# Kernel tuning notes

Measured on AMD Instinct MI355X. Metric: run time of the kernel, lower is better.

## Reference

```python
import jax, jax.numpy as jnp
import numpy as np
from jax import lax

B, T, H, L, IN = 256, 512, 128, 128, 3


def setup_inputs() -> dict:
    key = jax.random.key(0)
    ks = jax.random.split(key, 24)
    def n(k, shape, s=0.05):
        return jax.random.normal(k, shape, dtype=jnp.float32) * s
    lengths = jax.random.randint(ks[0], (B,), T // 2, T + 1)
    masks = (jnp.arange(T)[None, :] < lengths[:, None]).astype(jnp.int32)
    return {
        "x": n(ks[1], (B, T, IN), 1.0),
        "y": n(ks[2], (B, L, IN), 1.0),
        "masks": masks,
        "lengths": lengths,
        "W_ih0": n(ks[3], (4 * H, IN)), "W_hh0": n(ks[4], (4 * H, H)),
        "b_ih0": n(ks[5], (4 * H,)), "b_hh0": n(ks[6], (4 * H,)),
        "W_ih1": n(ks[7], (4 * H, H)), "W_hh1": n(ks[8], (4 * H, H)),
        "b_ih1": n(ks[9], (4 * H,)), "b_hh1": n(ks[10], (4 * H,)),
        "Wa": n(ks[11], (H, H)), "bWa": n(ks[12], (H,)),
        "Ua": n(ks[13], (H, H)), "bUa": n(ks[14], (H,)),
        "Va": n(ks[15], (H,)), "bVa": n(ks[16], (1,)),
        "fc1_w": n(ks[17], (32, H)), "fc1_b": n(ks[18], (32,)),
        "fc2_w": n(ks[19], (2, 32)), "fc2_b": n(ks[20], (2,)),
    }


def _lstm_cell(x_t, h, c, Wih, Whh, bih, bhh):
    # PyTorch gate order: i, f, g, o
    g = x_t @ Wih.T + h @ Whh.T + bih + bhh
    i, f, gg, o = jnp.split(g, 4, axis=-1)
    c = jax.nn.sigmoid(f) * c + jax.nn.sigmoid(i) * jnp.tanh(gg)
    h = jax.nn.sigmoid(o) * jnp.tanh(c)
    return h, c


def reference(x, y, masks, lengths,
              W_ih0, W_hh0, b_ih0, b_hh0,
              W_ih1, W_hh1, b_ih1, b_hh1,
              Wa, bWa, Ua, bUa, Va, bVa,
              fc1_w, fc1_b, fc2_w, fc2_b):
    Bn, Tn, _ = x.shape
    Ln = y.shape[1]
    Hn = W_hh0.shape[1]
    z = jnp.zeros((Bn, Hn), x.dtype)

    # ---- encoder: 2-layer LSTM with pack_padded semantics ----
    valid = (jnp.arange(Tn)[:, None] < lengths[None, :])[..., None]  # (T,B,1)

    def enc_step(carry, inp):
        h1, c1, h2, c2 = carry
        x_t, v = inp
        h1n, c1n = _lstm_cell(x_t, h1, c1, W_ih0, W_hh0, b_ih0, b_hh0)
        h2n, c2n = _lstm_cell(h1n, h2, c2, W_ih1, W_hh1, b_ih1, b_hh1)
        h1 = jnp.where(v, h1n, h1); c1 = jnp.where(v, c1n, c1)
        h2 = jnp.where(v, h2n, h2); c2 = jnp.where(v, c2n, c2)
        return (h1, c1, h2, c2), jnp.where(v, h2n, 0.0)

    (h1, c1, h2, c2), outs = lax.scan(enc_step, (z, z, z, z),
                                      (x.transpose(1, 0, 2), valid))
    lstm_out = outs.transpose(1, 0, 2)  # (B,T,H), zeros past length

    def attention(lo, h, m):
        s = jnp.tanh(lo @ Wa.T + bWa + (h @ Ua.T + bUa)[:, None, :])  # (B,T,H)
        scores = s @ Va + bVa  # (B,T)
        scores = jnp.where(m == 0, -jnp.inf, scores)
        w = jax.nn.softmax(scores, axis=1)
        return jnp.einsum('bt,btd->bd', w, lo)

    def head(ctx):
        return jax.nn.relu(ctx @ fc1_w.T + fc1_b) @ fc2_w.T + fc2_b

    out0 = head(attention(lstm_out, h2, masks))  # (B,2)

    # ---- decode loop (training=True, sampling_prob=1.0 -> pure teacher forcing) ----
    def dec_step(carry, inp):
        h1, c1, h2, c2, lo, m = carry
        y_t, i = inp
        h1, c1 = _lstm_cell(y_t, h1, c1, W_ih0, W_hh0, b_ih0, b_hh0)
        h2, c2 = _lstm_cell(h1, h2, c2, W_ih1, W_hh1, b_ih1, b_hh1)
        lo = lo.at[:, i + 1].set(h2)
        m = m.at[:, i + 1].set(1)
        out = head(attention(lo, h2, m))
        return (h1, c1, h2, c2, lo, m), out

    _, outs_dec = lax.scan(dec_step, (h1, c1, h2, c2, lstm_out, masks),
                           (y[:, :Ln - 1].transpose(1, 0, 2), jnp.arange(Ln - 1)))
    outputs = jnp.concatenate([out0[:, None, :], outs_dec.transpose(1, 0, 2)], axis=1)
    return outputs  # (B, L, 2)
```

## Files before the change

### kernel.cpp

```cpp
#include <hip/hip_runtime.h>

#define T 512
#define HDIM 128
#define LOUT 128
#define KEXT 639
#define KPAD 640
#define BM 4

typedef _Float16 half8 __attribute__((ext_vector_type(8)));
typedef _Float16 half4 __attribute__((ext_vector_type(4)));
typedef _Float16 half2t __attribute__((ext_vector_type(2)));
typedef float f32x4 __attribute__((ext_vector_type(4)));
typedef unsigned int u32x4 __attribute__((ext_vector_type(4)));

__device__ __forceinline__ int clampT(int v) { return v < 0 ? 0 : (v > T ? T : v); }

__device__ __forceinline__ half8 load8f(const float* p) {
  float4 q0 = *(const float4*)p;
  float4 q1 = *(const float4*)(p + 4);
  half8 v;
  v[0] = (_Float16)q0.x; v[1] = (_Float16)q0.y; v[2] = (_Float16)q0.z; v[3] = (_Float16)q0.w;
  v[4] = (_Float16)q1.x; v[5] = (_Float16)q1.y; v[6] = (_Float16)q1.z; v[7] = (_Float16)q1.w;
  return v;
}

__device__ __forceinline__ half8 load8h_once(const _Float16* p) {
  u32x4 raw = *(volatile const u32x4*)p;
  return __builtin_bit_cast(half8, raw);
}

__device__ __forceinline__ void cell_up(float gi, float gf, float gg, float go,
                                        float& cr, _Float16& hh, bool v) {
  const float A = 1.44269504f, B2 = 2.88539008f;
  const float Fi = __builtin_amdgcn_exp2f(-gi * A);
  const float Ff = __builtin_amdgcn_exp2f(-gf * A);
  const float Fo = __builtin_amdgcn_exp2f(-go * A);
  const float Eg = __builtin_amdgcn_exp2f(gg * B2);
  const float it = (Eg - 1.f) * __builtin_amdgcn_rcpf((1.f + Fi) * (1.f + Eg));
  const float cn = cr * __builtin_amdgcn_rcpf(1.f + Ff) + it;
  const float ec = __builtin_amdgcn_exp2f(-B2 * __builtin_fabsf(cn));
  const float h  = __builtin_copysignf(
      (1.f - ec) * __builtin_amdgcn_rcpf((1.f + Fo) * (1.f + ec)), cn);
  if (v) { cr = cn; hh = (_Float16)h; }
}

__device__ __forceinline__ float fast_tanh(float x) {
  float ax = __builtin_fabsf(x);
  float e = __builtin_amdgcn_exp2f(ax * -2.88539008f);
  float t = (1.f - e) * __builtin_amdgcn_rcpf(1.f + e);
  return __builtin_copysignf(t, x);
}

__global__ __launch_bounds__(256)
void prep_kernel(const float* __restrict__ Whh0, const float* __restrict__ Wih1,
                 const float* __restrict__ Whh1,
                 _Float16* __restrict__ A, _Float16* __restrict__ B,
                 _Float16* __restrict__ C)
{
  const int i = (blockIdx.x * 256 + threadIdx.x) * 4;
  float4 a = *(const float4*)(Whh0 + i);
  float4 b = *(const float4*)(Wih1 + i);
  float4 c = *(const float4*)(Whh1 + i);
  half4 ha = {(_Float16)a.x, (_Float16)a.y, (_Float16)a.z, (_Float16)a.w};
  half4 hb = {(_Float16)b.x, (_Float16)b.y, (_Float16)b.z, (_Float16)b.w};
  half4 hc = {(_Float16)c.x, (_Float16)c.y, (_Float16)c.z, (_Float16)c.w};
  *(half4*)(A + i) = ha;
  *(half4*)(B + i) = hb;
  *(half4*)(C + i) = hc;
}

__global__ __launch_bounds__(512) __attribute__((amdgpu_waves_per_eu(1, 2)))
void lstm_kernel(const float* __restrict__ x, const float* __restrict__ y,
                 const int* __restrict__ lengths,
                 const float* __restrict__ Wih0,
                 const _Float16* __restrict__ Wh0h,
                 const _Float16* __restrict__ Wi1h,
                 const _Float16* __restrict__ Wh1h,
                 const float* __restrict__ bih0, const float* __restrict__ bhh0,
                 const float* __restrict__ bih1, const float* __restrict__ bhh1,
                 _Float16* __restrict__ Vext, _Float16* __restrict__ Hfin)
{
  const int tid  = threadIdx.x;
  const int w    = tid >> 6;
  const int lane = tid & 63;
  const int fr   = lane & 15;
  const int fg   = lane >> 4;
  const int b0   = blockIdx.x * BM;
  const int u    = w * 16 + fr;
  const int wpos   = (u >> 3) * 144 + fg * 8 + (u & 7);
  const int frbase = (fr >> 2) * 8;

  __shared__ _Float16 h1buf[2][2304];
  __shared__ _Float16 h2buf[2][2304];
  __shared__ float    xlds[T][BM][3];
  __shared__ float    ylds[LOUT][BM][3];
  __shared__ float    w0lds[512][3];
  __shared__ float    b0lds[512], b1lds[512];
  __shared__ int      lens_s[BM];

  half8 wh0[4][4], wi1[4][4], wh1[4][4];
#pragma unroll
  for (int g = 0; g < 4; ++g) {
    const int n = g * 128 + u;
#pragma unroll
    for (int kf = 0; kf < 4; ++kf) {
      const int off = n * HDIM + kf * 32 + fg * 8;
      wh0[g][kf] = load8h_once(Wh0h + off);
      wi1[g][kf] = load8h_once(Wi1h + off);
      wh1[g][kf] = load8h_once(Wh1h + off);
    }
  }

  if (tid < BM) lens_s[tid] = clampT(lengths[b0 + tid]);
  {
    const int n = tid;
    b0lds[n] = bih0[n] + bhh0[n];
    b1lds[n] = bih1[n] + bhh1[n];
    w0lds[n][0] = Wih0[n * 3 + 0];
    w0lds[n][1] = Wih0[n * 3 + 1];
    w0lds[n][2] = Wih0[n * 3 + 2];
  }
  for (int it = tid; it < 2304; it += 512) {
    h1buf[0][it] = (_Float16)0.f; h1buf[1][it] = (_Float16)0.f;
    h2buf[0][it] = (_Float16)0.f; h2buf[1][it] = (_Float16)0.f;
  }
  for (int it = tid; it < BM * T * 3; it += 512) {
    const int b = it / (T * 3), r = it - b * (T * 3);
    xlds[r / 3][b][r % 3] = x[(size_t)(b0 + b) * T * 3 + r];
  }
  for (int it = tid; it < BM * LOUT * 3; it += 512) {
    const int b = it / (LOUT * 3), r = it - b * (LOUT * 3);
    ylds[r / 3][b][r % 3] = y[(size_t)(b0 + b) * LOUT * 3 + r];
  }
  __syncthreads();

  const int mylen_l = lens_s[fg];
  int maxlen = 0;
#pragma unroll
  for (int i = 0; i < BM; ++i) maxlen = max(maxlen, lens_s[i]);
  const int S = maxlen + LOUT - 1;

  for (int t = mylen_l; t < T; ++t)
    Vext[((size_t)(b0 + fg) * KEXT + t) * HDIM + u] = (_Float16)0.f;

  float c1r = 0.f, c2r = 0.f;
  _Float16 h1h = (_Float16)0.f, h2h = (_Float16)0.f, h2p = (_Float16)0.f;
  {
    const float x0 = xlds[0][fg][0], x1 = xlds[0][fg][1], x2 = xlds[0][fg][2];
    float gv[4];
#pragma unroll
    for (int g = 0; g < 4; ++g) {
      const int n = g * 128 + u;
      gv[g] = b0lds[n] + x0 * w0lds[n][0] + x1 * w0lds[n][1] + x2 * w0lds[n][2];
    }
    cell_up(gv[0], gv[1], gv[2], gv[3], c1r, h1h, true);
    h1buf[0][wpos] = h1h;
  }
  __syncthreads();

  for (int s = 0; s < S; ++s) {
    const int p = s & 1;
    if (s > 0) {
      const int ps = s - 1;
      if ((ps >= maxlen) || (ps < mylen_l)) {
        const int orow = (ps < maxlen) ? ps : (T + ps - maxlen);
        Vext[((size_t)(b0 + fg) * KEXT + orow) * HDIM + u] = h2p;
      }
      if (ps == maxlen - 1)
        Hfin[(size_t)(b0 + fg) * HDIM + u] = h2p;
    }
    half8 h1f[4], h2f[4];
#pragma unroll
    for (int kf = 0; kf < 4; ++kf) {
      const int roff = (kf * 4 + fg) * 144 + frbase;
      h1f[kf] = *(const half8*)&h1buf[p][roff];
      h2f[kf] = *(const half8*)&h2buf[p ^ 1][roff];
    }
    float gv[4];
#pragma unroll
    for (int g = 0; g < 4; ++g) {
      f32x4 a = {0.f, 0.f, 0.f, 0.f};
#pragma unroll
      for (int kf = 0; kf < 4; ++kf)
        a = __builtin_amdgcn_mfma_f32_16x16x32_f16(h1f[kf], wi1[g][kf], a, 0, 0, 0);
#pragma unroll
      for (int kf = 0; kf < 4; ++kf)
        a = __builtin_amdgcn_mfma_f32_16x16x32_f16(h2f[kf], wh1[g][kf], a, 0, 0, 0);
      gv[g] = a[0] + b1lds[g * 128 + u];
    }
    {
      const bool v1 = (s >= maxlen) || (s < mylen_l);
      cell_up(gv[0], gv[1], gv[2], gv[3], c2r, h2h, v1);
      h2buf[p][wpos] = h2h;
      h2p = h2h;
    }
    if (s + 1 < S) {
#pragma unroll
      for (int g = 0; g < 4; ++g) {
        f32x4 a = {0.f, 0.f, 0.f, 0.f};
#pragma unroll
        for (int kf = 0; kf < 4; ++kf)
          a = __builtin_amdgcn_mfma_f32_16x16x32_f16(h1f[kf], wh0[g][kf], a, 0, 0, 0);
        gv[g] = a[0];
      }
      const int k = s + 1;
      const float* xp = (k < maxlen) ? &xlds[k][fg][0] : &ylds[k - maxlen][fg][0];
      const float x0 = xp[0], x1 = xp[1], x2 = xp[2];
#pragma unroll
      for (int g = 0; g < 4; ++g) {
        const int n = g * 128 + u;
        gv[g] += b0lds[n] + x0 * w0lds[n][0] + x1 * w0lds[n][1] + x2 * w0lds[n][2];
      }
      const bool v0 = (k >= maxlen) || (k < mylen_l);
      cell_up(gv[0], gv[1], gv[2], gv[3], c1r, h1h, v0);
      h1buf[p ^ 1][wpos] = h1h;
    }
    __syncthreads();
  }
  {
    const int orow = T + (S - 1) - maxlen;
    Vext[((size_t)(b0 + fg) * KEXT + orow) * HDIM + u] = h2p;
  }
}

__global__ __launch_bounds__(256, 1)
void proj_kernel(const _Float16* __restrict__ Vext, const _Float16* __restrict__ Hfin,
                 const float* __restrict__ Wa, const float* __restrict__ bWa,
                 const float* __restrict__ Ua, const float* __restrict__ bUa,
                 _Float16* __restrict__ tA, _Float16* __restrict__ tq)
{
  const int b = blockIdx.x;
  const int tid = threadIdx.x;
  const int wave = tid >> 6, lane = tid & 63;
  const int fr = lane & 15, fg = lane >> 4;
  __shared__ _Float16 tile[4][128][24];

  half8 bf[8][4];
  float bias_r[8];
#pragma unroll
  for (int nt = 0; nt < 8; ++nt) {
    const int ho = nt * 16 + fr;
    bias_r[nt] = bWa[ho];
#pragma unroll
    for (int kf = 0; kf < 4; ++kf)
      bf[nt][kf] = load8f(Wa + ho * HDIM + kf * 32 + fg * 8);
  }

  for (int r = 0; r < 10; ++r) {
    const int mt = r * 4 + wave;
    int row = mt * 16 + fr;
    if (row > KEXT - 1) row = KEXT - 1;
    const _Float16* src = Vext + ((size_t)b * KEXT + row) * HDIM;
    half8 af[4];
#pragma unroll
    for (int kf = 0; kf < 4; ++kf) af[kf] = *(const half8*)(src + kf * 32 + fg * 8);
#pragma unroll
    for (int nt = 0; nt < 8; ++nt) {
      f32x4 a = {0.f, 0.f, 0.f, 0.f};
#pragma unroll
      for (int kf = 0; kf < 4; ++kf)
        a = __builtin_amdgcn_mfma_f32_16x16x32_f16(af[kf], bf[nt][kf], a, 0, 0, 0);
#pragma unroll
      for (int j = 0; j < 4; ++j)
        tile[wave][nt * 16 + fr][fg * 4 + j] = (_Float16)fast_tanh(a[j] + bias_r[nt]);
    }
    __syncthreads();
    for (int it = tid; it < 4 * 128; it += 256) {
      const int w2 = it >> 7, ho = it & 127;
      const half8 v0 = *(const half8*)&tile[w2][ho][0];
      const half8 v1 = *(const half8*)&tile[w2][ho][8];
      _Float16* dst = tA + ((size_t)b * HDIM + ho) * KPAD + (r * 4 + w2) * 16;
      *(half8*)dst = v0;
      *(half8*)(dst + 8) = v1;
    }
    __syncthreads();
  }

#pragma unroll
  for (int nt = 0; nt < 8; ++nt) {
    const int ho = nt * 16 + fr;
    bias_r[nt] = bUa[ho];
#pragma unroll
    for (int kf = 0; kf < 4; ++kf)
      bf[nt][kf] = load8f(Ua + ho * HDIM + kf * 32 + fg * 8);
  }
  for (int r = 0; r < 2; ++r) {
    const int mt = r * 4 + wave;
    const int prow = mt * 16 + fr;
    const _Float16* src = (prow == 0)
        ? (Hfin + (size_t)b * HDIM)
        : (Vext + ((size_t)b * KEXT + 511 + prow) * HDIM);
    half8 af[4];
#pragma unroll
    for (int kf = 0; kf < 4; ++kf) af[kf] = *(const half8*)(src + kf * 32 + fg * 8);
#pragma unroll
    for (int nt = 0; nt < 8; ++nt) {
      f32x4 a = {0.f, 0.f, 0.f, 0.f};
#pragma unroll
      for (int kf = 0; kf < 4; ++kf)
        a = __builtin_amdgcn_mfma_f32_16x16x32_f16(af[kf], bf[nt][kf], a, 0, 0, 0);
#pragma unroll
      for (int j = 0; j < 4; ++j) {
        const int pq = mt * 16 + fg * 4 + j;
        tq[((size_t)b * LOUT + pq) * HDIM + nt * 16 + fr] = (_Float16)fast_tanh(a[j] + bias_r[nt]);
      }
    }
  }
}

__global__ __launch_bounds__(512)
void attn_kernel(const _Float16* __restrict__ Vext,
                 const _Float16* __restrict__ tA,
                 const _Float16* __restrict__ tq,
                 const float* __restrict__ Va,
                 const int* __restrict__ lengths,
                 const float* __restrict__ fc1w, const float* __restrict__ fc1b,
                 const float* __restrict__ fc2w, const float* __restrict__ fc2b,
                 float* __restrict__ out)
{
  const int b = blockIdx.x;
  const int p0 = blockIdx.y * 16;
  const int tid = threadIdx.x, wv = tid >> 6, lane = tid & 63;

  __shared__ __align__(16) char stg_raw[128 * 136 * 2];
  __shared__ __align__(16) char sc_raw[16 * 648 * 2];
  __shared__ __align__(16) _Float16 qs16[16][136];
  __shared__ float vas[HDIM];
  auto stg = (_Float16(*)[136])stg_raw;
  auto sc  = (_Float16(*)[648])sc_raw;

  for (int it = tid; it < 256; it += 512)
    *(half8*)&qs16[it >> 4][(it & 15) * 8] =
        *(const half8*)(tq + ((size_t)b * LOUT + p0 + (it >> 4)) * HDIM + (it & 15) * 8);
  if (tid < HDIM) vas[tid] = Va[tid];
  const int len = clampT(lengths[b]);
  const float fb   = (lane < 32) ? fc1b[lane] : 0.f;
  const float w2a  = (lane < 32) ? fc2w[lane] : 0.f;
  const float w2b  = (lane < 32) ? fc2w[32 + lane] : 0.f;
  const float f2b0 = fc2b[0], f2b1 = fc2b[1];
  const _Float16 NEGINF = (_Float16)(-__builtin_inff());
  const half2t one2 = {(_Float16)1.f, (_Float16)1.f};
  __syncthreads();

  for (int kc = 0; kc < 5; ++kc) {
    const int ck0 = kc * 128;
    const bool alive = (ck0 < T) ? ((ck0 == 0) || (ck0 < len))
                                 : ((ck0 - T) < p0 + 15);
    if (alive) {
      __syncthreads();
      for (int it = tid; it < 2048; it += 512) {
        const int hh = it >> 4, ks = it & 15;
        *(half8*)&stg[hh][ks * 8] =
            *(const half8*)(tA + ((size_t)b * HDIM + hh) * KPAD + ck0 + ks * 8);
      }
      __syncthreads();
    }
#pragma unroll
    for (int pp = 0; pp < 2; ++pp) {
      const int prow = wv * 2 + pp;
      const int p = p0 + prow;
      const int k0 = ck0 + lane * 2, k1 = k0 + 1;
      bool anyv;
      if (ck0 < T) {
        const int kmax = min(ck0 + 127, len - 1);
        anyv = (ck0 == 0) || ((ck0 < len) && (kmax > p));
      } else {
        anyv = (ck0 - T) < p;
      }
      if (!anyv) {
        half2t z; z[0] = NEGINF; z[1] = NEGINF;
        *(half2t*)&sc[prow][k0] = z;
        continue;
      }
      float acc0 = 0.f, acc1 = 0.f;
#pragma unroll 4
      for (int h = 0; h < HDIM; ++h) {
        const half2t a = *(const half2t*)&stg[h][lane * 2];
        const _Float16 qh = qs16[prow][h];
        half2t q2; q2[0] = qh; q2[1] = qh;
        const half2t aq = a * q2;
        const half2t s2 = a + q2;
        const half2t x2 = aq * aq;
        const half2t x4 = x2 * x2;
        const half2t om = one2 - aq;
        const half2t f1 = s2 * om;
        const half2t f2 = f1 * x2 + f1;
        const half2t f3 = f2 * x4 + f2;
        const float va = vas[h];
        acc0 = fmaf(va, (float)f3[0], acc0);
        acc1 = fmaf(va, (float)f3[1], acc1);
      }
      const bool v0 = (k0 < T) ? ((k0 < len) && (k0 == 0 || k0 > p)) : ((k0 - T) < p);
      const bool v1 = (k1 < T) ? ((k1 < len) && (k1 > p)) : ((k1 - T) < p);
      half2t sv;
      sv[0] = v0 ? (_Float16)acc0 : NEGINF;
      sv[1] = v1 ? (_Float16)acc1 : NEGINF;
      *(half2t*)&sc[prow][k0] = sv;
    }
  }

  float inv[2];
#pragma unroll
  for (int pp = 0; pp < 2; ++pp) {
    const int prow = wv * 2 + pp;
    float m = -__builtin_inff();
    for (int k = lane; k < KPAD; k += 64) m = fmaxf(m, (float)sc[prow][k]);
#pragma unroll
    for (int off = 32; off; off >>= 1) m = fmaxf(m, __shfl_xor(m, off, 64));
    float ssum = 0.f;
    for (int k = lane; k < KPAD; k += 64) {
      const float e = __builtin_amdgcn_exp2f(((float)sc[prow][k] - m) * 1.44269504f);
      sc[prow][k] = (_Float16)e;
      ssum += e;
    }
#pragma unroll
    for (int off = 32; off; off >>= 1) ssum += __shfl_xor(ssum, off, 64);
    inv[pp] = __builtin_amdgcn_rcpf(ssum);
  }

  float ca[2] = {0.f, 0.f}, cb[2] = {0.f, 0.f};
  for (int vc = 0; vc < 5; ++vc) {
    const int ck0 = vc * 128;
    const bool alive = (ck0 < T) ? ((ck0 == 0) || (ck0 < len))
                                 : ((ck0 - T) < p0 + 15);
    if (!alive) continue;
    __syncthreads();
    for (int it = tid; it < 2048; it += 512) {
      const int kk = it >> 4, hs = it & 15;
      const int krow = min(ck0 + kk, KEXT - 1);
      *(half8*)&stg[kk][hs * 8] =
          *(const half8*)(Vext + ((size_t)b * KEXT + krow) * HDIM + hs * 8);
    }
    __syncthreads();
#pragma unroll
    for (int pp = 0; pp < 2; ++pp) {
      const int prow = wv * 2 + pp;
      const int p = p0 + prow;
      bool anyv;
      if (ck0 < T) {
        const int kmax = min(ck0 + 127, len - 1);
        anyv = (ck0 == 0) || ((ck0 < len) && (kmax > p));
      } else {
        anyv = (ck0 - T) < p;
      }
      if (!anyv) continue;
      float a0 = ca[pp], a1 = cb[pp];
#pragma unroll 4
      for (int kk = 0; kk < 128; ++kk) {
        const float wgt = (float)sc[prow][ck0 + kk];
        const half2t v = *(const half2t*)&stg[kk][lane * 2];
        a0 = fmaf(wgt, (float)v[0], a0);
        a1 = fmaf(wgt, (float)v[1], a1);
      }
      ca[pp] = a0; cb[pp] = a1;
    }
  }
  __syncthreads();

  auto ctxs = (float(*)[128])sc_raw;
  auto f1w  = (_Float16(*)[132])stg_raw;
#pragma unroll
  for (int pp = 0; pp < 2; ++pp) {
    const int prow = wv * 2 + pp;
    float2 cv; cv.x = ca[pp] * inv[pp]; cv.y = cb[pp] * inv[pp];
    *(float2*)&ctxs[prow][lane * 2] = cv;
  }
  for (int it = tid; it < 32 * HDIM; it += 512)
    f1w[it >> 7][it & 127] = (_Float16)fc1w[it];
  __syncthreads();

#pragma unroll
  for (int pp = 0; pp < 2; ++pp) {
    const int prow = wv * 2 + pp;
    float r = 0.f;
    if (lane < 32) {
      float a = fb;
      for (int h = 0; h < HDIM; ++h)
        a = fmaf(ctxs[prow][h], (float)f1w[lane][h], a);
      r = fmaxf(a, 0.f);
    }
    float s0 = r * w2a, s1 = r * w2b;
#pragma unroll
    for (int off = 16; off; off >>= 1) {
      s0 += __shfl_xor(s0, off, 64);
      s1 += __shfl_xor(s1, off, 64);
    }
    if (lane == 0) {
      float* o = out + ((size_t)b * LOUT + p0 + prow) * 2;
      o[0] = s0 + f2b0;
      o[1] = s1 + f2b1;
    }
  }
}

extern "C" void kernel_launch(void* const* d_in, const int* in_sizes, int n_in,
                              void* d_out, int out_size, void* d_ws, size_t ws_size,
                              hipStream_t stream)
{
  const float* x     = (const float*)d_in[0];
  const float* y     = (const float*)d_in[1];
  const int* lengths = (const int*)d_in[3];
  const float* Wih0  = (const float*)d_in[4];
  const float* Whh0  = (const float*)d_in[5];
  const float* bih0  = (const float*)d_in[6];
  const float* bhh0  = (const float*)d_in[7];
  const float* Wih1  = (const float*)d_in[8];
  const float* Whh1  = (const float*)d_in[9];
  const float* bih1  = (const float*)d_in[10];
  const float* bhh1  = (const float*)d_in[11];
  const float* Wa    = (const float*)d_in[12];
  const float* bWa   = (const float*)d_in[13];
  const float* Ua    = (const float*)d_in[14];
  const float* bUa   = (const float*)d_in[15];
  const float* Va    = (const float*)d_in[16];
  const float* fc1w  = (const float*)d_in[18];
  const float* fc1b  = (const float*)d_in[19];
  const float* fc2w  = (const float*)d_in[20];
  const float* fc2b  = (const float*)d_in[21];

  char* wsp = (char*)d_ws;
  _Float16* Vext  = (_Float16*)(wsp);
  _Float16* Hfin  = (_Float16*)(wsp + 41877504);
  _Float16* tA    = (_Float16*)(wsp + 41943040);
  _Float16* tq    = (_Float16*)(wsp + 83886080);
  _Float16* W16_0 = (_Float16*)(wsp + 92274688);
  _Float16* W16_i = (_Float16*)(wsp + 92405760);
  _Float16* W16_1 = (_Float16*)(wsp + 92536832);
  (void)in_sizes; (void)n_in; (void)out_size; (void)ws_size;

  prep_kernel<<<64, 256, 0, stream>>>(Whh0, Wih1, Whh1, W16_0, W16_i, W16_1);
  lstm_kernel<<<64, 512, 0, stream>>>(x, y, lengths, Wih0, W16_0, W16_i, W16_1,
                                      bih0, bhh0, bih1, bhh1, Vext, Hfin);
  proj_kernel<<<256, 256, 0, stream>>>(Vext, Hfin, Wa, bWa, Ua, bUa, tA, tq);
  attn_kernel<<<dim3(256, 8), 512, 0, stream>>>(Vext, tA, tq, Va, lengths,
                                                fc1w, fc1b, fc2w, fc2b,
                                                (float*)d_out);
}
```

Baseline: 1.567 ms.

## Use MFMA for attention context, transpose values, vectorize score dot products

Replaces the scalar per-lane weighted sum over values with a 16x16x32 MFMA over softmax weights and a transposed value matrix. A new vt_kernel produces that transposed copy. tA is now stored k-major with an XOR-swizzled shared tile, and the tanh-approximation score is computed on half8 vectors with fdot2 against an f16 Va. The cost is an extra kernel launch and an extra write and read of the transposed values. Folding Va into fp16 and accumulating through fdot2 slightly changes rounding.

After: 1.271 ms. 1.23x faster.

```diff
diff --git a/kernel.cpp b/kernel.cpp
--- a/kernel.cpp
+++ b/kernel.cpp
@@ -49,6 +49,23 @@
   float e = __builtin_amdgcn_exp2f(ax * -2.88539008f);
   float t = (1.f - e) * __builtin_amdgcn_rcpf(1.f + e);
   return __builtin_copysignf(t, x);
+}
+
+__device__ __forceinline__ float dotf3(half8 a, half8 q, half8 v, float acc) {
+  half8 aq = a * q;
+  half8 s2 = a + q;
+  half8 x2 = aq * aq;
+  half8 x4 = x2 * x2;
+  half8 f1 = s2 - s2 * aq;
+  half8 f2 = f1 * x2 + f1;
+  half8 f3 = f2 * x4 + f2;
+  const half2t* fp = (const half2t*)&f3;
+  const half2t* vp = (const half2t*)&v;
+  acc = __builtin_amdgcn_fdot2(fp[0], vp[0], acc, false);
+  acc = __builtin_amdgcn_fdot2(fp[1], vp[1], acc, false);
+  acc = __builtin_amdgcn_fdot2(fp[2], vp[2], acc, false);
+  acc = __builtin_amdgcn_fdot2(fp[3], vp[3], acc, false);
+  return acc;
 }
 
 __global__ __launch_bounds__(256)
@@ -233,7 +250,6 @@
   const int tid = threadIdx.x;
   const int wave = tid >> 6, lane = tid & 63;
   const int fr = lane & 15, fg = lane >> 4;
-  __shared__ _Float16 tile[4][128][24];
 
   half8 bf[8][4];
   float bias_r[8];
@@ -261,19 +277,12 @@
       for (int kf = 0; kf < 4; ++kf)
         a = __builtin_amdgcn_mfma_f32_16x16x32_f16(af[kf], bf[nt][kf], a, 0, 0, 0);
 #pragma unroll
-      for (int j = 0; j < 4; ++j)
-        tile[wave][nt * 16 + fr][fg * 4 + j] = (_Float16)fast_tanh(a[j] + bias_r[nt]);
-    }
-    __syncthreads();
-    for (int it = tid; it < 4 * 128; it += 256) {
-      const int w2 = it >> 7, ho = it & 127;
-      const half8 v0 = *(const half8*)&tile[w2][ho][0];
-      const half8 v1 = *(const half8*)&tile[w2][ho][8];
-      _Float16* dst = tA + ((size_t)b * HDIM + ho) * KPAD + (r * 4 + w2) * 16;
-      *(half8*)dst = v0;
-      *(half8*)(dst + 8) = v1;
-    }
-    __syncthreads();
+      for (int j = 0; j < 4; ++j) {
+        const int ko = mt * 16 + fg * 4 + j;
+        tA[((size_t)b * KPAD + ko) * HDIM + nt * 16 + fr] =
+            (_Float16)fast_tanh(a[j] + bias_r[nt]);
+      }
+    }
   }
 
 #pragma unroll
@@ -308,8 +317,30 @@
   }
 }
 
+__global__ __launch_bounds__(256)
+void vt_kernel(const _Float16* __restrict__ Vext, _Float16* __restrict__ VT)
+{
+  const int b = blockIdx.x, kt = blockIdx.y;
+  const int tid = threadIdx.x;
+  __shared__ _Float16 tile[64][136];
+  for (int it = tid; it < 1024; it += 256) {
+    const int kl = it >> 4, hs = it & 15;
+    const int krow = min(kt * 64 + kl, KEXT - 1);
+    *(half8*)&tile[kl][hs * 8] =
+        *(const half8*)(Vext + ((size_t)b * KEXT + krow) * HDIM + hs * 8);
+  }
+  __syncthreads();
+  for (int it = tid; it < 1024; it += 256) {
+    const int h = it >> 3, ks = (it & 7) * 8;
+    half8 v;
+#pragma unroll
+    for (int e = 0; e < 8; ++e) v[e] = tile[ks + e][h];
+    *(half8*)(VT + ((size_t)b * HDIM + h) * KPAD + kt * 64 + ks) = v;
+  }
+}
+
 __global__ __launch_bounds__(512)
-void attn_kernel(const _Float16* __restrict__ Vext,
+void attn_kernel(const _Float16* __restrict__ VT,
                  const _Float16* __restrict__ tA,
                  const _Float16* __restrict__ tq,
                  const float* __restrict__ Va,
@@ -322,24 +353,22 @@
   const int p0 = blockIdx.y * 16;
   const int tid = threadIdx.x, wv = tid >> 6, lane = tid & 63;
 
-  __shared__ __align__(16) char stg_raw[128 * 136 * 2];
-  __shared__ __align__(16) char sc_raw[16 * 648 * 2];
+  __shared__ __align__(16) _Float16 stgS[128 * 136];
+  __shared__ __align__(16) _Float16 sc[16 * 656];
   __shared__ __align__(16) _Float16 qs16[16][136];
-  __shared__ float vas[HDIM];
-  auto stg = (_Float16(*)[136])stg_raw;
-  auto sc  = (_Float16(*)[648])sc_raw;
+  __shared__ __align__(16) _Float16 vva[128];
+  __shared__ float invs[16];
 
   for (int it = tid; it < 256; it += 512)
     *(half8*)&qs16[it >> 4][(it & 15) * 8] =
         *(const half8*)(tq + ((size_t)b * LOUT + p0 + (it >> 4)) * HDIM + (it & 15) * 8);
-  if (tid < HDIM) vas[tid] = Va[tid];
+  if (tid < 128) vva[tid] = (_Float16)Va[tid];
   const int len = clampT(lengths[b]);
   const float fb   = (lane < 32) ? fc1b[lane] : 0.f;
   const float w2a  = (lane < 32) ? fc2w[lane] : 0.f;
   const float w2b  = (lane < 32) ? fc2w[32 + lane] : 0.f;
   const float f2b0 = fc2b[0], f2b1 = fc2b[1];
   const _Float16 NEGINF = (_Float16)(-__builtin_inff());
-  const half2t one2 = {(_Float16)1.f, (_Float16)1.f};
   __syncthreads();
 
   for (int kc = 0; kc < 5; ++kc) {
@@ -349,9 +378,10 @@
     if (alive) {
       __syncthreads();
       for (int it = tid; it < 2048; it += 512) {
-        const int hh = it >> 4, ks = it & 15;
-        *(half8*)&stg[hh][ks * 8] =
-            *(const half8*)(tA + ((size_t)b * HDIM + hh) * KPAD + ck0 + ks * 8);
+        const int k = it >> 4, hs = it & 15;
+        const int off = k * 136 + ((hs * 8) ^ (((k >> 1) & 7) << 3));
+        *(half8*)&stgS[off] =
+            *(const half8*)(tA + ((size_t)b * KPAD + ck0 + k) * HDIM + hs * 8);
       }
       __syncthreads();
     }
@@ -369,103 +399,70 @@
       }
       if (!anyv) {
         half2t z; z[0] = NEGINF; z[1] = NEGINF;
-        *(half2t*)&sc[prow][k0] = z;
+        *(half2t*)&sc[prow * 656 + k0] = z;
         continue;
       }
       float acc0 = 0.f, acc1 = 0.f;
+      const int base0 = (lane * 2) * 136;
+      const int base1 = base0 + 136;
+      const int sw = (lane & 7) << 3;
 #pragma unroll 4
-      for (int h = 0; h < HDIM; ++h) {
-        const half2t a = *(const half2t*)&stg[h][lane * 2];
-        const _Float16 qh = qs16[prow][h];
-        half2t q2; q2[0] = qh; q2[1] = qh;
-        const half2t aq = a * q2;
-        const half2t s2 = a + q2;
-        const half2t x2 = aq * aq;
-        const half2t x4 = x2 * x2;
-        const half2t om = one2 - aq;
-        const half2t f1 = s2 * om;
-        const half2t f2 = f1 * x2 + f1;
-        const half2t f3 = f2 * x4 + f2;
-        const float va = vas[h];
-        acc0 = fmaf(va, (float)f3[0], acc0);
-        acc1 = fmaf(va, (float)f3[1], acc1);
+      for (int hb = 0; hb < 16; ++hb) {
+        const int ho = (hb * 8) ^ sw;
+        const half8 a0 = *(const half8*)&stgS[base0 + ho];
+        const half8 a1 = *(const half8*)&stgS[base1 + ho];
+        const half8 q8 = *(const half8*)&qs16[prow][hb * 8];
+        const half8 v8 = *(const half8*)&vva[hb * 8];
+        acc0 = dotf3(a0, q8, v8, acc0);
+        acc1 = dotf3(a1, q8, v8, acc1);
       }
       const bool v0 = (k0 < T) ? ((k0 < len) && (k0 == 0 || k0 > p)) : ((k0 - T) < p);
       const bool v1 = (k1 < T) ? ((k1 < len) && (k1 > p)) : ((k1 - T) < p);
       half2t sv;
       sv[0] = v0 ? (_Float16)acc0 : NEGINF;
       sv[1] = v1 ? (_Float16)acc1 : NEGINF;
-      *(half2t*)&sc[prow][k0] = sv;
-    }
-  }
-
-  float inv[2];
+      *(half2t*)&sc[prow * 656 + k0] = sv;
+    }
+  }
+
 #pragma unroll
   for (int pp = 0; pp < 2; ++pp) {
     const int prow = wv * 2 + pp;
     float m = -__builtin_inff();
-    for (int k = lane; k < KPAD; k += 64) m = fmaxf(m, (float)sc[prow][k]);
+    for (int k = lane; k < KPAD; k += 64) m = fmaxf(m, (float)sc[prow * 656 + k]);
 #pragma unroll
     for (int off = 32; off; off >>= 1) m = fmaxf(m, __shfl_xor(m, off, 64));
     float ssum = 0.f;
     for (int k = lane; k < KPAD; k += 64) {
-      const float e = __builtin_amdgcn_exp2f(((float)sc[prow][k] - m) * 1.44269504f);
-      sc[prow][k] = (_Float16)e;
+      const float e = __builtin_amdgcn_exp2f(((float)sc[prow * 656 + k] - m) * 1.44269504f);
+      sc[prow * 656 + k] = (_Float16)e;
       ssum += e;
     }
 #pragma unroll
     for (int off = 32; off; off >>= 1) ssum += __shfl_xor(ssum, off, 64);
-    inv[pp] = __builtin_amdgcn_rcpf(ssum);
-  }
-
-  float ca[2] = {0.f, 0.f}, cb[2] = {0.f, 0.f};
-  for (int vc = 0; vc < 5; ++vc) {
-    const int ck0 = vc * 128;
-    const bool alive = (ck0 < T) ? ((ck0 == 0) || (ck0 < len))
-                                 : ((ck0 - T) < p0 + 15);
-    if (!alive) continue;
-    __syncthreads();
-    for (int it = tid; it < 2048; it += 512) {
-      const int kk = it >> 4, hs = it & 15;
-      const int krow = min(ck0 + kk, KEXT - 1);
-      *(half8*)&stg[kk][hs * 8] =
-          *(const half8*)(Vext + ((size_t)b * KEXT + krow) * HDIM + hs * 8);
-    }
-    __syncthreads();
-#pragma unroll
-    for (int pp = 0; pp < 2; ++pp) {
-      const int prow = wv * 2 + pp;
-      const int p = p0 + prow;
-      bool anyv;
-      if (ck0 < T) {
-        const int kmax = min(ck0 + 127, len - 1);
-        anyv = (ck0 == 0) || ((ck0 < len) && (kmax > p));
-      } else {
-        anyv = (ck0 - T) < p;
-      }
-      if (!anyv) continue;
-      float a0 = ca[pp], a1 = cb[pp];
+    if (lane == 0) invs[prow] = __builtin_amdgcn_rcpf(ssum);
+  }
+  __syncthreads();
+
+  const int fr = lane & 15, fg = lane >> 4;
+  const int hcol = wv * 16 + fr;
+  f32x4 cac = {0.f, 0.f, 0.f, 0.f};
+  const _Float16* vtrow = VT + ((size_t)b * HDIM + hcol) * KPAD;
 #pragma unroll 4
-      for (int kk = 0; kk < 128; ++kk) {
-        const float wgt = (float)sc[prow][ck0 + kk];
-        const half2t v = *(const half2t*)&stg[kk][lane * 2];
-        a0 = fmaf(wgt, (float)v[0], a0);
-        a1 = fmaf(wgt, (float)v[1], a1);
-      }
-      ca[pp] = a0; cb[pp] = a1;
-    }
-  }
-  __syncthreads();
-
-  auto ctxs = (float(*)[128])sc_raw;
-  auto f1w  = (_Float16(*)[132])stg_raw;
-#pragma unroll
-  for (int pp = 0; pp < 2; ++pp) {
-    const int prow = wv * 2 + pp;
-    float2 cv; cv.x = ca[pp] * inv[pp]; cv.y = cb[pp] * inv[pp];
-    *(float2*)&ctxs[prow][lane * 2] = cv;
-  }
-  for (int it = tid; it < 32 * HDIM; it += 512)
+  for (int kk = 0; kk < 20; ++kk) {
+    const half8 av = *(const half8*)&sc[fr * 656 + kk * 32 + fg * 8];
+    const half8 bv = *(const half8*)(vtrow + kk * 32 + fg * 8);
+    cac = __builtin_amdgcn_mfma_f32_16x16x32_f16(av, bv, cac, 0, 0, 0);
+  }
+
+  auto ctxs = (float(*)[132])stgS;
+  auto f1w  = (_Float16(*)[136])(stgS + 4224);
+#pragma unroll
+  for (int j = 0; j < 4; ++j) {
+    const int pr = fg * 4 + j;
+    ctxs[pr][hcol] = cac[j] * invs[pr];
+  }
+  for (int it = tid; it < 4096; it += 512)
     f1w[it >> 7][it & 127] = (_Float16)fc1w[it];
   __syncthreads();
 
@@ -526,13 +523,15 @@
   _Float16* W16_0 = (_Float16*)(wsp + 92274688);
   _Float16* W16_i = (_Float16*)(wsp + 92405760);
   _Float16* W16_1 = (_Float16*)(wsp + 92536832);
+  _Float16* VT    = (_Float16*)(wsp + 92667904);
   (void)in_sizes; (void)n_in; (void)out_size; (void)ws_size;
 
   prep_kernel<<<64, 256, 0, stream>>>(Whh0, Wih1, Whh1, W16_0, W16_i, W16_1);
   lstm_kernel<<<64, 512, 0, stream>>>(x, y, lengths, Wih0, W16_0, W16_i, W16_1,
                                       bih0, bhh0, bih1, bhh1, Vext, Hfin);
   proj_kernel<<<256, 256, 0, stream>>>(Vext, Hfin, Wa, bWa, Ua, bUa, tA, tq);
-  attn_kernel<<<dim3(256, 8), 512, 0, stream>>>(Vext, tA, tq, Va, lengths,
+  vt_kernel<<<dim3(256, 10), 256, 0, stream>>>(Vext, VT);
+  attn_kernel<<<dim3(256, 8), 512, 0, stream>>>(VT, tA, tq, Va, lengths,
                                                 fc1w, fc1b, fc2w, fc2b,
                                                 (float*)d_out);
 }
```
